# Performance work log

Measured on AMD Instinct MI355X. Metric: run time of the kernel, lower is better.

The kernel has to match this reference:

```python
import jax, jax.numpy as jnp
import numpy as np

N, DQ, T, H1 = 131072, 256, 4, 512

def setup_inputs() -> dict:
    key = jax.random.key(0)
    k_q, k_w0, k_b0, k_w1, k_z = jax.random.split(key, 5)
    return {
        "q": jax.random.normal(k_q, (N, DQ), dtype=jnp.float32),
        "Z": jax.random.randint(k_z, (N,), 0, T, dtype=jnp.int32),
        "W0": jax.random.normal(k_w0, (T, DQ, H1), dtype=jnp.float32) * (1.0 / np.sqrt(DQ)),
        "b0": jax.random.normal(k_b0, (T, H1), dtype=jnp.float32) * 0.01,
        "W1": jax.random.normal(k_w1, (T, H1), dtype=jnp.float32) * (1.0 / np.sqrt(H1)),
        "b1": jnp.zeros((), dtype=jnp.float32),
    }

def reference(q, Z, W0, b0, W1, b1):
    # Dense grouped-GEMM over all T types (T is small), then select per-atom
    # type result. Avoids materializing the per-atom [N, dq, h1] gathered
    # weight tensor that tf.gather would create.
    h_all = jnp.einsum('nd,tdh->nth', q, W0)              # [N, T, H1]
    h = jnp.take_along_axis(h_all, Z[:, None, None].astype(jnp.int32), axis=1)[:, 0, :]  # [N, H1]
    h = jnp.tanh(h + b0[Z])                               # hidden activations
    F = jnp.einsum('nh,nh->n', h, W1[Z]) + b1             # [N]
    return F
```

## Files before the change

### kernel.cpp

```cpp
#include <hip/hip_runtime.h>
#include <hip/hip_bf16.h>

#define N_ATOMS 131072
#define DQ 256
#define H1 512
#define NTYPES 4
#define TILE_M 64
#define NPAD (N_ATOMS + NTYPES * TILE_M)
#define MTILES ((N_ATOMS / TILE_M) + NTYPES)

typedef __bf16 bf16x8 __attribute__((ext_vector_type(8)));
typedef float f32x16 __attribute__((ext_vector_type(16)));

__device__ __forceinline__ unsigned short f2bf(float f) {
  unsigned int u = __builtin_bit_cast(unsigned int, f);
  u += 0x7fffu + ((u >> 16) & 1u);
  return (unsigned short)(u >> 16);
}

__device__ __forceinline__ float fast_tanh(float x) {
  float e = __expf(2.0f * x);
  return 1.0f - 2.0f * __builtin_amdgcn_rcpf(e + 1.0f);
}

__global__ __launch_bounds__(256) void prep_kernel(
    const float* __restrict__ W0, const int* __restrict__ Z,
    unsigned short* __restrict__ W0s, int* __restrict__ perm,
    int* __restrict__ blockcounts)
{
  const int b = blockIdx.x, tid = threadIdx.x;
  const int gid = b * 256 + tid;

  for (int i = gid; i < NPAD; i += 512 * 256) perm[i] = -1;

  if (gid < NTYPES * (DQ / 8) * H1) {
    const int n  = gid & (H1 - 1);
    const int kg = (gid >> 9) & 31;
    const int t  = gid >> 14;
    const float* src = W0 + ((size_t)(t * DQ + kg * 8) * H1 + n);
    unsigned short o[8];
#pragma unroll
    for (int j = 0; j < 8; ++j) o[j] = f2bf(src[(size_t)j * H1]);
    uint4 v;
    v.x = (unsigned)o[0] | ((unsigned)o[1] << 16);
    v.y = (unsigned)o[2] | ((unsigned)o[3] << 16);
    v.z = (unsigned)o[4] | ((unsigned)o[5] << 16);
    v.w = (unsigned)o[6] | ((unsigned)o[7] << 16);
    ((uint4*)W0s)[gid] = v;
  }

  __shared__ int lc[NTYPES];
  if (tid < NTYPES) lc[tid] = 0;
  __syncthreads();
  atomicAdd(&lc[Z[gid]], 1);
  __syncthreads();
  if (tid < NTYPES) blockcounts[b * NTYPES + tid] = lc[tid];
}

__global__ __launch_bounds__(256) void scan_kernel(
    const int* __restrict__ blockcounts, int* __restrict__ padded_off,
    int* __restrict__ cursors)
{
  __shared__ int sums[NTYPES];
  const int tid = threadIdx.x;
  if (tid < NTYPES) sums[tid] = 0;
  __syncthreads();
  const int t = tid & 3;
  int acc = 0;
  for (int b = tid >> 2; b < 512; b += 64) acc += blockcounts[b * 4 + t];
  atomicAdd(&sums[t], acc);
  __syncthreads();
  if (tid == 0) {
    int off = 0;
#pragma unroll
    for (int i = 0; i < NTYPES; ++i) {
      padded_off[i] = off;
      cursors[i] = off;
      off += (sums[i] + TILE_M - 1) & ~(TILE_M - 1);
    }
    padded_off[NTYPES] = off;
  }
}

__global__ __launch_bounds__(256) void scatter_kernel(
    const int* __restrict__ Z, int* __restrict__ cursors, int* __restrict__ perm)
{
  __shared__ int lc[NTYPES], lbase[NTYPES];
  const int tid = threadIdx.x;
  const int gid = blockIdx.x * 256 + tid;
  if (tid < NTYPES) lc[tid] = 0;
  __syncthreads();
  const int t  = Z[gid];
  const int my = atomicAdd(&lc[t], 1);
  __syncthreads();
  if (tid < NTYPES) lbase[tid] = lc[tid] ? atomicAdd(&cursors[tid], lc[tid]) : 0;
  __syncthreads();
  perm[lbase[t] + my] = gid;
}

__global__ __launch_bounds__(256, 2) void gemm_kernel(
    const float* __restrict__ q, const int* __restrict__ perm,
    const int* __restrict__ padded_off, const unsigned short* __restrict__ W0s,
    const float* __restrict__ b0, const float* __restrict__ W1,
    const float* __restrict__ b1p, float* __restrict__ out)
{
  __shared__ unsigned short Alds[(DQ / 8) * TILE_M * 8];
  __shared__ float Fws[4][TILE_M];

  const int gr0 = blockIdx.x * TILE_M;
  if (gr0 >= padded_off[NTYPES]) return;
  int t = 0;
#pragma unroll
  for (int i = 1; i < NTYPES; ++i) t += (gr0 >= padded_off[i]) ? 1 : 0;

  const int tid = threadIdx.x;

  {
    const int row = tid >> 2, c4 = tid & 3;
    const int atom = perm[gr0 + row];
    const float* qrow = q + (size_t)(atom < 0 ? 0 : atom) * DQ;
#pragma unroll
    for (int i = 0; i < 16; ++i) {
      const int k = c4 * 64 + i * 4;
      float4 v = make_float4(0.f, 0.f, 0.f, 0.f);
      if (atom >= 0) v = *(const float4*)(qrow + k);
      ushort4 o;
      o.x = f2bf(v.x); o.y = f2bf(v.y); o.z = f2bf(v.z); o.w = f2bf(v.w);
      *(ushort4*)&Alds[((k >> 3) * TILE_M + row) * 8 + (k & 7)] = o;
    }
  }
  __syncthreads();

  const int l = tid & 63, w = tid >> 6;
  const int half = l >> 5, ln = l & 31;

  f32x16 acc[2][4];
#pragma unroll
  for (int mt = 0; mt < 2; ++mt)
#pragma unroll
    for (int nt = 0; nt < 4; ++nt) acc[mt][nt] = (f32x16)0.0f;

  const unsigned short* Bt = W0s + (size_t)t * (DQ * H1);
  const unsigned short* Bbase = Bt + (size_t)(w * 128 + ln) * 8;

#pragma unroll 4
  for (int step = 0; step < 16; ++step) {
    const int kg = 2 * step + half;
    const bf16x8 a0 = *(const bf16x8*)&Alds[(kg * TILE_M + ln) * 8];
    const bf16x8 a1 = *(const bf16x8*)&Alds[(kg * TILE_M + 32 + ln) * 8];
    const unsigned short* bp = Bbase + (size_t)kg * (H1 * 8);
    const bf16x8 b0f = *(const bf16x8*)(bp);
    const bf16x8 b1f = *(const bf16x8*)(bp + 32 * 8);
    const bf16x8 b2f = *(const bf16x8*)(bp + 64 * 8);
    const bf16x8 b3f = *(const bf16x8*)(bp + 96 * 8);
    acc[0][0] = __builtin_amdgcn_mfma_f32_32x32x16_bf16(a0, b0f, acc[0][0], 0, 0, 0);
    acc[1][0] = __builtin_amdgcn_mfma_f32_32x32x16_bf16(a1, b0f, acc[1][0], 0, 0, 0);
    acc[0][1] = __builtin_amdgcn_mfma_f32_32x32x16_bf16(a0, b1f, acc[0][1], 0, 0, 0);
    acc[1][1] = __builtin_amdgcn_mfma_f32_32x32x16_bf16(a1, b1f, acc[1][1], 0, 0, 0);
    acc[0][2] = __builtin_amdgcn_mfma_f32_32x32x16_bf16(a0, b2f, acc[0][2], 0, 0, 0);
    acc[1][2] = __builtin_amdgcn_mfma_f32_32x32x16_bf16(a1, b2f, acc[1][2], 0, 0, 0);
    acc[0][3] = __builtin_amdgcn_mfma_f32_32x32x16_bf16(a0, b3f, acc[0][3], 0, 0, 0);
    acc[1][3] = __builtin_amdgcn_mfma_f32_32x32x16_bf16(a1, b3f, acc[1][3], 0, 0, 0);
  }

  float b0v[4], w1v[4];
#pragma unroll
  for (int nt = 0; nt < 4; ++nt) {
    const int c = w * 128 + nt * 32 + ln;
    b0v[nt] = b0[t * H1 + c];
    w1v[nt] = W1[t * H1 + c];
  }
#pragma unroll
  for (int mt = 0; mt < 2; ++mt) {
#pragma unroll
    for (int r = 0; r < 16; ++r) {
      float s = 0.f;
#pragma unroll
      for (int nt = 0; nt < 4; ++nt)
        s += w1v[nt] * fast_tanh(acc[mt][nt][r] + b0v[nt]);
      s += __shfl_xor(s, 1);
      s += __shfl_xor(s, 2);
      s += __shfl_xor(s, 4);
      s += __shfl_xor(s, 8);
      s += __shfl_xor(s, 16);
      if (ln == 0)
        Fws[w][mt * 32 + (r & 3) + 8 * (r >> 2) + 4 * half] = s;
    }
  }
  __syncthreads();

  if (tid < TILE_M) {
    const int atom = perm[gr0 + tid];
    if (atom >= 0)
      out[atom] = Fws[0][tid] + Fws[1][tid] + Fws[2][tid] + Fws[3][tid] + b1p[0];
  }
}

extern "C" void kernel_launch(void* const* d_in, const int* in_sizes, int n_in,
                              void* d_out, int out_size, void* d_ws, size_t ws_size,
                              hipStream_t stream) {
  const float* q  = (const float*)d_in[0];
  const int*   Z  = (const int*)d_in[1];
  const float* W0 = (const float*)d_in[2];
  const float* b0 = (const float*)d_in[3];
  const float* W1 = (const float*)d_in[4];
  const float* b1 = (const float*)d_in[5];
  float* out = (float*)d_out;

  char* ws = (char*)d_ws;
  int* blockcounts = (int*)(ws);
  int* padded_off  = (int*)(ws + 8192);
  int* cursors     = (int*)(ws + 8192 + 32);
  int* perm        = (int*)(ws + 8192 + 64);
  unsigned short* W0s = (unsigned short*)(ws + 8192 + 64 + (size_t)NPAD * 4);

  hipLaunchKernelGGL(prep_kernel,    dim3(512),    dim3(256), 0, stream, W0, Z, W0s, perm, blockcounts);
  hipLaunchKernelGGL(scan_kernel,    dim3(1),      dim3(256), 0, stream, blockcounts, padded_off, cursors);
  hipLaunchKernelGGL(scatter_kernel, dim3(512),    dim3(256), 0, stream, Z, cursors, perm);
  hipLaunchKernelGGL(gemm_kernel,    dim3(MTILES), dim3(256), 0, stream, q, perm, padded_off, W0s, b0, W1, b1, out);
}
```

Before: 281.4 us.

## Split GEMM N-dimension into two passes to cut accumulators and raise occupancy

```diff
diff --git a/kernel.cpp b/kernel.cpp
--- a/kernel.cpp
+++ b/kernel.cpp
@@ -98,14 +98,14 @@
   perm[lbase[t] + my] = gid;
 }
 
-__global__ __launch_bounds__(256, 2) void gemm_kernel(
+__global__ __launch_bounds__(256, 4) void gemm_kernel(
     const float* __restrict__ q, const int* __restrict__ perm,
     const int* __restrict__ padded_off, const unsigned short* __restrict__ W0s,
     const float* __restrict__ b0, const float* __restrict__ W1,
     const float* __restrict__ b1p, float* __restrict__ out)
 {
   __shared__ unsigned short Alds[(DQ / 8) * TILE_M * 8];
-  __shared__ float Fws[4][TILE_M];
+  __shared__ float Fws[16][TILE_M];
 
   const int gr0 = blockIdx.x * TILE_M;
   if (gr0 >= padded_off[NTYPES]) return;
@@ -134,65 +134,67 @@
   const int l = tid & 63, w = tid >> 6;
   const int half = l >> 5, ln = l & 31;
 
-  f32x16 acc[2][4];
-#pragma unroll
-  for (int mt = 0; mt < 2; ++mt)
-#pragma unroll
-    for (int nt = 0; nt < 4; ++nt) acc[mt][nt] = (f32x16)0.0f;
-
   const unsigned short* Bt = W0s + (size_t)t * (DQ * H1);
-  const unsigned short* Bbase = Bt + (size_t)(w * 128 + ln) * 8;
-
-#pragma unroll 4
-  for (int step = 0; step < 16; ++step) {
-    const int kg = 2 * step + half;
-    const bf16x8 a0 = *(const bf16x8*)&Alds[(kg * TILE_M + ln) * 8];
-    const bf16x8 a1 = *(const bf16x8*)&Alds[(kg * TILE_M + 32 + ln) * 8];
-    const unsigned short* bp = Bbase + (size_t)kg * (H1 * 8);
-    const bf16x8 b0f = *(const bf16x8*)(bp);
-    const bf16x8 b1f = *(const bf16x8*)(bp + 32 * 8);
-    const bf16x8 b2f = *(const bf16x8*)(bp + 64 * 8);
-    const bf16x8 b3f = *(const bf16x8*)(bp + 96 * 8);
-    acc[0][0] = __builtin_amdgcn_mfma_f32_32x32x16_bf16(a0, b0f, acc[0][0], 0, 0, 0);
-    acc[1][0] = __builtin_amdgcn_mfma_f32_32x32x16_bf16(a1, b0f, acc[1][0], 0, 0, 0);
-    acc[0][1] = __builtin_amdgcn_mfma_f32_32x32x16_bf16(a0, b1f, acc[0][1], 0, 0, 0);
-    acc[1][1] = __builtin_amdgcn_mfma_f32_32x32x16_bf16(a1, b1f, acc[1][1], 0, 0, 0);
-    acc[0][2] = __builtin_amdgcn_mfma_f32_32x32x16_bf16(a0, b2f, acc[0][2], 0, 0, 0);
-    acc[1][2] = __builtin_amdgcn_mfma_f32_32x32x16_bf16(a1, b2f, acc[1][2], 0, 0, 0);
-    acc[0][3] = __builtin_amdgcn_mfma_f32_32x32x16_bf16(a0, b3f, acc[0][3], 0, 0, 0);
-    acc[1][3] = __builtin_amdgcn_mfma_f32_32x32x16_bf16(a1, b3f, acc[1][3], 0, 0, 0);
-  }
-
-  float b0v[4], w1v[4];
-#pragma unroll
-  for (int nt = 0; nt < 4; ++nt) {
-    const int c = w * 128 + nt * 32 + ln;
-    b0v[nt] = b0[t * H1 + c];
-    w1v[nt] = W1[t * H1 + c];
-  }
-#pragma unroll
-  for (int mt = 0; mt < 2; ++mt) {
-#pragma unroll
-    for (int r = 0; r < 16; ++r) {
-      float s = 0.f;
-#pragma unroll
-      for (int nt = 0; nt < 4; ++nt)
-        s += w1v[nt] * fast_tanh(acc[mt][nt][r] + b0v[nt]);
-      s += __shfl_xor(s, 1);
-      s += __shfl_xor(s, 2);
-      s += __shfl_xor(s, 4);
-      s += __shfl_xor(s, 8);
-      s += __shfl_xor(s, 16);
-      if (ln == 0)
-        Fws[w][mt * 32 + (r & 3) + 8 * (r >> 2) + 4 * half] = s;
+
+#pragma unroll
+  for (int p = 0; p < 2; ++p) {
+    f32x16 acc[2][2];
+#pragma unroll
+    for (int mt = 0; mt < 2; ++mt)
+#pragma unroll
+      for (int nt = 0; nt < 2; ++nt) acc[mt][nt] = (f32x16)0.0f;
+
+    const unsigned short* Bbase = Bt + (size_t)(p * 256 + w * 64 + ln) * 8;
+
+#pragma unroll 2
+    for (int step = 0; step < 16; ++step) {
+      const int kg = 2 * step + half;
+      const bf16x8 a0 = *(const bf16x8*)&Alds[(kg * TILE_M + ln) * 8];
+      const bf16x8 a1 = *(const bf16x8*)&Alds[(kg * TILE_M + 32 + ln) * 8];
+      const unsigned short* bp = Bbase + (size_t)kg * (H1 * 8);
+      const bf16x8 bf0 = *(const bf16x8*)(bp);
+      const bf16x8 bf1 = *(const bf16x8*)(bp + 32 * 8);
+      acc[0][0] = __builtin_amdgcn_mfma_f32_32x32x16_bf16(a0, bf0, acc[0][0], 0, 0, 0);
+      acc[1][0] = __builtin_amdgcn_mfma_f32_32x32x16_bf16(a1, bf0, acc[1][0], 0, 0, 0);
+      acc[0][1] = __builtin_amdgcn_mfma_f32_32x32x16_bf16(a0, bf1, acc[0][1], 0, 0, 0);
+      acc[1][1] = __builtin_amdgcn_mfma_f32_32x32x16_bf16(a1, bf1, acc[1][1], 0, 0, 0);
+    }
+
+    float b0v[2], w1v[2];
+#pragma unroll
+    for (int nt = 0; nt < 2; ++nt) {
+      const int c = p * 256 + w * 64 + nt * 32 + ln;
+      b0v[nt] = b0[t * H1 + c];
+      w1v[nt] = W1[t * H1 + c];
+    }
+#pragma unroll
+    for (int mt = 0; mt < 2; ++mt) {
+#pragma unroll
+      for (int r = 0; r < 16; ++r) {
+        float s = w1v[0] * fast_tanh(acc[mt][0][r] + b0v[0])
+                + w1v[1] * fast_tanh(acc[mt][1][r] + b0v[1]);
+        s += __shfl_xor(s, 1);
+        s += __shfl_xor(s, 2);
+        s += __shfl_xor(s, 4);
+        if ((l & 7) == 0) {
+          const int row  = mt * 32 + (r & 3) + 8 * (r >> 2) + 4 * half;
+          const int slot = w * 4 + ((l >> 3) & 3);
+          if (p == 0) Fws[slot][row] = s;
+          else        Fws[slot][row] += s;
+        }
+      }
     }
   }
   __syncthreads();
 
   if (tid < TILE_M) {
     const int atom = perm[gr0 + tid];
-    if (atom >= 0)
-      out[atom] = Fws[0][tid] + Fws[1][tid] + Fws[2][tid] + Fws[3][tid] + b1p[0];
+    if (atom >= 0) {
+      float s = 0.f;
+#pragma unroll
+      for (int i = 0; i < 16; ++i) s += Fws[i][tid];
+      out[atom] = s + b1p[0];
+    }
   }
 }
 
```

Result: slower. 296.0 us (+5.2%).

## Add persistent double-buffered GEMM with async LDS loads of pre-converted bf16 q

Applied to the files above, without the earlier changes.

```diff
diff --git a/kernel.cpp b/kernel.cpp
--- a/kernel.cpp
+++ b/kernel.cpp
@@ -12,6 +12,13 @@
 typedef __bf16 bf16x8 __attribute__((ext_vector_type(8)));
 typedef float f32x16 __attribute__((ext_vector_type(16)));
 
+typedef __attribute__((address_space(3))) unsigned int lds_u32_t;
+typedef __attribute__((address_space(1))) const unsigned int glb_u32_t;
+
+__device__ __forceinline__ void async16(const void* g, void* l) {
+  __builtin_amdgcn_global_load_lds((glb_u32_t*)g, (lds_u32_t*)l, 16, 0, 0);
+}
+
 __device__ __forceinline__ unsigned short f2bf(float f) {
   unsigned int u = __builtin_bit_cast(unsigned int, f);
   u += 0x7fffu + ((u >> 16) & 1u);
@@ -24,9 +31,10 @@
 }
 
 __global__ __launch_bounds__(256) void prep_kernel(
-    const float* __restrict__ W0, const int* __restrict__ Z,
-    unsigned short* __restrict__ W0s, int* __restrict__ perm,
-    int* __restrict__ blockcounts)
+    const float* __restrict__ W0, const float* __restrict__ qf,
+    const int* __restrict__ Z, unsigned short* __restrict__ W0s,
+    unsigned short* __restrict__ qb, int* __restrict__ perm,
+    int* __restrict__ blockcounts, int qconv)
 {
   const int b = blockIdx.x, tid = threadIdx.x;
   const int gid = b * 256 + tid;
@@ -55,6 +63,15 @@
   atomicAdd(&lc[Z[gid]], 1);
   __syncthreads();
   if (tid < NTYPES) blockcounts[b * NTYPES + tid] = lc[tid];
+
+  if (qconv) {
+    for (int i = gid; i < (N_ATOMS * DQ) / 4; i += 512 * 256) {
+      const float4 v = ((const float4*)qf)[i];
+      ushort4 o;
+      o.x = f2bf(v.x); o.y = f2bf(v.y); o.z = f2bf(v.z); o.w = f2bf(v.w);
+      ((ushort4*)qb)[i] = o;
+    }
+  }
 }
 
 __global__ __launch_bounds__(256) void scan_kernel(
@@ -96,6 +113,119 @@
   if (tid < NTYPES) lbase[tid] = lc[tid] ? atomicAdd(&cursors[tid], lc[tid]) : 0;
   __syncthreads();
   perm[lbase[t] + my] = gid;
+}
+
+__global__ __launch_bounds__(256, 2) void gemm_persist(
+    const unsigned short* __restrict__ qb, const int* __restrict__ perm,
+    const int* __restrict__ padded_off, const unsigned short* __restrict__ W0s,
+    const float* __restrict__ b0, const float* __restrict__ W1,
+    const float* __restrict__ b1p, float* __restrict__ out)
+{
+  __shared__ unsigned short Alds[2][DQ / 8][TILE_M][8];
+  __shared__ float Fws[2][4][TILE_M];
+
+  const int tid = threadIdx.x;
+  const int l = tid & 63, w = tid >> 6;
+  const int half = l >> 5, ln = l & 31;
+  const int bx = (int)blockIdx.x;
+
+  const int po1 = padded_off[1], po2 = padded_off[2], po3 = padded_off[3];
+  const int po4 = padded_off[4];
+  const int NT = po4 / TILE_M;
+  const int ntile = 4 + ((bx < NT - 2048) ? 1 : 0);
+  const float b1v = b1p[0];
+
+  {
+    const int a0 = perm[bx * TILE_M + l];
+    const unsigned short* src = qb + (size_t)(a0 < 0 ? 0 : a0) * DQ;
+#pragma unroll
+    for (int i = 0; i < 8; ++i)
+      async16(src + (w * 8 + i) * 8, &Alds[0][w * 8 + i][0][0]);
+  }
+  int atomn = (ntile > 1) ? perm[(bx + 512) * TILE_M + l] : 0;
+  __syncthreads();
+
+  for (int it = 0; it < ntile; ++it) {
+    const int cur = it & 1;
+    const int tcur = (it < 4) ? bx + it * 512 : 2048 + bx;
+    const int gr0 = tcur * TILE_M;
+    const int t = ((gr0 >= po1) ? 1 : 0) + ((gr0 >= po2) ? 1 : 0)
+                + ((gr0 >= po3) ? 1 : 0);
+
+    f32x16 acc[2][4];
+#pragma unroll
+    for (int mt = 0; mt < 2; ++mt)
+#pragma unroll
+      for (int nt = 0; nt < 4; ++nt) acc[mt][nt] = (f32x16)0.0f;
+
+    const unsigned short* Bt = W0s + (size_t)t * (DQ * H1);
+    const unsigned short* Bbase = Bt + (size_t)(w * 128 + ln) * 8;
+
+#pragma unroll 4
+    for (int step = 0; step < 16; ++step) {
+      const int kg = 2 * step + half;
+      const bf16x8 a0 = *(const bf16x8*)&Alds[cur][kg][ln][0];
+      const bf16x8 a1 = *(const bf16x8*)&Alds[cur][kg][32 + ln][0];
+      const unsigned short* bp = Bbase + (size_t)kg * (H1 * 8);
+      const bf16x8 b0f = *(const bf16x8*)(bp);
+      const bf16x8 b1f = *(const bf16x8*)(bp + 32 * 8);
+      const bf16x8 b2f = *(const bf16x8*)(bp + 64 * 8);
+      const bf16x8 b3f = *(const bf16x8*)(bp + 96 * 8);
+      acc[0][0] = __builtin_amdgcn_mfma_f32_32x32x16_bf16(a0, b0f, acc[0][0], 0, 0, 0);
+      acc[1][0] = __builtin_amdgcn_mfma_f32_32x32x16_bf16(a1, b0f, acc[1][0], 0, 0, 0);
+      acc[0][1] = __builtin_amdgcn_mfma_f32_32x32x16_bf16(a0, b1f, acc[0][1], 0, 0, 0);
+      acc[1][1] = __builtin_amdgcn_mfma_f32_32x32x16_bf16(a1, b1f, acc[1][1], 0, 0, 0);
+      acc[0][2] = __builtin_amdgcn_mfma_f32_32x32x16_bf16(a0, b2f, acc[0][2], 0, 0, 0);
+      acc[1][2] = __builtin_amdgcn_mfma_f32_32x32x16_bf16(a1, b2f, acc[1][2], 0, 0, 0);
+      acc[0][3] = __builtin_amdgcn_mfma_f32_32x32x16_bf16(a0, b3f, acc[0][3], 0, 0, 0);
+      acc[1][3] = __builtin_amdgcn_mfma_f32_32x32x16_bf16(a1, b3f, acc[1][3], 0, 0, 0);
+    }
+
+    float b0v[4], w1v[4];
+#pragma unroll
+    for (int nt = 0; nt < 4; ++nt) {
+      const int c = w * 128 + nt * 32 + ln;
+      b0v[nt] = b0[t * H1 + c];
+      w1v[nt] = W1[t * H1 + c];
+    }
+
+    if (it + 1 < ntile) {
+      const unsigned short* srcn = qb + (size_t)(atomn < 0 ? 0 : atomn) * DQ;
+#pragma unroll
+      for (int i = 0; i < 8; ++i)
+        async16(srcn + (w * 8 + i) * 8, &Alds[cur ^ 1][w * 8 + i][0][0]);
+      if (it + 2 < ntile) {
+        const int tnn = (it + 2 < 4) ? bx + (it + 2) * 512 : 2048 + bx;
+        atomn = perm[tnn * TILE_M + l];
+      }
+    }
+
+#pragma unroll
+    for (int mt = 0; mt < 2; ++mt) {
+#pragma unroll
+      for (int r = 0; r < 16; ++r) {
+        float s = 0.f;
+#pragma unroll
+        for (int nt = 0; nt < 4; ++nt)
+          s += w1v[nt] * fast_tanh(acc[mt][nt][r] + b0v[nt]);
+        s += __shfl_xor(s, 1);
+        s += __shfl_xor(s, 2);
+        s += __shfl_xor(s, 4);
+        s += __shfl_xor(s, 8);
+        s += __shfl_xor(s, 16);
+        if (ln == 0)
+          Fws[cur][w][mt * 32 + (r & 3) + 8 * (r >> 2) + 4 * half] = s;
+      }
+    }
+    __syncthreads();
+
+    if (tid < TILE_M) {
+      const int a = perm[gr0 + tid];
+      if (a >= 0)
+        out[a] = Fws[cur][0][tid] + Fws[cur][1][tid] + Fws[cur][2][tid]
+               + Fws[cur][3][tid] + b1v;
+    }
+  }
 }
 
 __global__ __launch_bounds__(256, 2) void gemm_kernel(
@@ -114,7 +244,6 @@
   for (int i = 1; i < NTYPES; ++i) t += (gr0 >= padded_off[i]) ? 1 : 0;
 
   const int tid = threadIdx.x;
-
   {
     const int row = tid >> 2, c4 = tid & 3;
     const int atom = perm[gr0 + row];
@@ -214,8 +343,22 @@
   int* perm        = (int*)(ws + 8192 + 64);
   unsigned short* W0s = (unsigned short*)(ws + 8192 + 64 + (size_t)NPAD * 4);
 
-  hipLaunchKernelGGL(prep_kernel,    dim3(512),    dim3(256), 0, stream, W0, Z, W0s, perm, blockcounts);
-  hipLaunchKernelGGL(scan_kernel,    dim3(1),      dim3(256), 0, stream, blockcounts, padded_off, cursors);
-  hipLaunchKernelGGL(scatter_kernel, dim3(512),    dim3(256), 0, stream, Z, cursors, perm);
-  hipLaunchKernelGGL(gemm_kernel,    dim3(MTILES), dim3(256), 0, stream, q, perm, padded_off, W0s, b0, W1, b1, out);
-}
+  const size_t qb_off = ((8192 + 64 + (size_t)NPAD * 4
+                        + (size_t)NTYPES * DQ * H1 * 2) + 511) & ~(size_t)511;
+  const size_t need = qb_off + (size_t)N_ATOMS * DQ * 2;
+  const int use_persist = (ws_size >= need) ? 1 : 0;
+  unsigned short* qb = (unsigned short*)(ws + qb_off);
+
+  hipLaunchKernelGGL(prep_kernel, dim3(512), dim3(256), 0, stream,
+                     W0, q, Z, W0s, qb, perm, blockcounts, use_persist);
+  hipLaunchKernelGGL(scan_kernel, dim3(1), dim3(256), 0, stream,
+                     blockcounts, padded_off, cursors);
+  hipLaunchKernelGGL(scatter_kernel, dim3(512), dim3(256), 0, stream,
+                     Z, cursors, perm);
+  if (use_persist)
+    hipLaunchKernelGGL(gemm_persist, dim3(512), dim3(256), 0, stream,
+                       qb, perm, padded_off, W0s, b0, W1, b1, out);
+  else
+    hipLaunchKernelGGL(gemm_kernel, dim3(MTILES), dim3(256), 0, stream,
+                       q, perm, padded_off, W0s, b0, W1, b1, out);
+}
```

After: 303.6 us. +7.9%, slower.

## Merge bucketing kernels and make GEMM persistent with double-buffered tile prefetch

Applied to the files above, without the earlier changes.

```diff
diff --git a/kernel.cpp b/kernel.cpp
--- a/kernel.cpp
+++ b/kernel.cpp
@@ -6,8 +6,6 @@
 #define H1 512
 #define NTYPES 4
 #define TILE_M 64
-#define NPAD (N_ATOMS + NTYPES * TILE_M)
-#define MTILES ((N_ATOMS / TILE_M) + NTYPES)
 
 typedef __bf16 bf16x8 __attribute__((ext_vector_type(8)));
 typedef float f32x16 __attribute__((ext_vector_type(16)));
@@ -23,15 +21,17 @@
   return 1.0f - 2.0f * __builtin_amdgcn_rcpf(e + 1.0f);
 }
 
+__global__ __launch_bounds__(64) void init_kernel(int* __restrict__ hdr) {
+  if (threadIdx.x < 16) hdr[threadIdx.x] = 0;
+}
+
 __global__ __launch_bounds__(256) void prep_kernel(
     const float* __restrict__ W0, const int* __restrict__ Z,
     unsigned short* __restrict__ W0s, int* __restrict__ perm,
-    int* __restrict__ blockcounts)
+    int* __restrict__ cnt)
 {
   const int b = blockIdx.x, tid = threadIdx.x;
   const int gid = b * 256 + tid;
-
-  for (int i = gid; i < NPAD; i += 512 * 256) perm[i] = -1;
 
   if (gid < NTYPES * (DQ / 8) * H1) {
     const int n  = gid & (H1 - 1);
@@ -49,151 +49,176 @@
     ((uint4*)W0s)[gid] = v;
   }
 
-  __shared__ int lc[NTYPES];
-  if (tid < NTYPES) lc[tid] = 0;
-  __syncthreads();
-  atomicAdd(&lc[Z[gid]], 1);
-  __syncthreads();
-  if (tid < NTYPES) blockcounts[b * NTYPES + tid] = lc[tid];
-}
-
-__global__ __launch_bounds__(256) void scan_kernel(
-    const int* __restrict__ blockcounts, int* __restrict__ padded_off,
-    int* __restrict__ cursors)
-{
-  __shared__ int sums[NTYPES];
-  const int tid = threadIdx.x;
-  if (tid < NTYPES) sums[tid] = 0;
-  __syncthreads();
-  const int t = tid & 3;
-  int acc = 0;
-  for (int b = tid >> 2; b < 512; b += 64) acc += blockcounts[b * 4 + t];
-  atomicAdd(&sums[t], acc);
-  __syncthreads();
-  if (tid == 0) {
-    int off = 0;
-#pragma unroll
-    for (int i = 0; i < NTYPES; ++i) {
-      padded_off[i] = off;
-      cursors[i] = off;
-      off += (sums[i] + TILE_M - 1) & ~(TILE_M - 1);
-    }
-    padded_off[NTYPES] = off;
-  }
-}
-
-__global__ __launch_bounds__(256) void scatter_kernel(
-    const int* __restrict__ Z, int* __restrict__ cursors, int* __restrict__ perm)
-{
   __shared__ int lc[NTYPES], lbase[NTYPES];
-  const int tid = threadIdx.x;
-  const int gid = blockIdx.x * 256 + tid;
   if (tid < NTYPES) lc[tid] = 0;
   __syncthreads();
   const int t  = Z[gid];
   const int my = atomicAdd(&lc[t], 1);
   __syncthreads();
-  if (tid < NTYPES) lbase[tid] = lc[tid] ? atomicAdd(&cursors[tid], lc[tid]) : 0;
-  __syncthreads();
-  perm[lbase[t] + my] = gid;
-}
-
-__global__ __launch_bounds__(256, 2) void gemm_kernel(
+  if (tid < NTYPES) lbase[tid] = lc[tid] ? atomicAdd(&cnt[tid], lc[tid]) : 0;
+  __syncthreads();
+  perm[t * N_ATOMS + lbase[t] + my] = gid;
+}
+
+__device__ __forceinline__ void issue_loads(float4* st, const float* q,
+                                            int atom, int c4) {
+  const float* qrow = q + (size_t)atom * DQ + c4 * 64;
+#pragma unroll
+  for (int i = 0; i < 16; ++i) st[i] = *(const float4*)(qrow + i * 4);
+}
+
+__device__ __forceinline__ void convert_store(
+    const float4* st, unsigned short (*A)[TILE_M][8], int row, int c4) {
+#pragma unroll
+  for (int i2 = 0; i2 < 8; ++i2) {
+    const int k = c4 * 64 + i2 * 8;
+    uint4 vv;
+    vv.x = (unsigned)f2bf(st[2*i2].x)     | ((unsigned)f2bf(st[2*i2].y)   << 16);
+    vv.y = (unsigned)f2bf(st[2*i2].z)     | ((unsigned)f2bf(st[2*i2].w)   << 16);
+    vv.z = (unsigned)f2bf(st[2*i2+1].x)   | ((unsigned)f2bf(st[2*i2+1].y) << 16);
+    vv.w = (unsigned)f2bf(st[2*i2+1].z)   | ((unsigned)f2bf(st[2*i2+1].w) << 16);
+    *(uint4*)&A[k >> 3][row][0] = vv;
+  }
+}
+
+__global__ __launch_bounds__(256, 2) void gemm_persist(
     const float* __restrict__ q, const int* __restrict__ perm,
-    const int* __restrict__ padded_off, const unsigned short* __restrict__ W0s,
-    const float* __restrict__ b0, const float* __restrict__ W1,
+    const int* __restrict__ cnt, int* __restrict__ ticket,
+    const unsigned short* __restrict__ W0s,
+    const float* __restrict__ b0g, const float* __restrict__ W1,
     const float* __restrict__ b1p, float* __restrict__ out)
 {
-  __shared__ unsigned short Alds[(DQ / 8) * TILE_M * 8];
-  __shared__ float Fws[4][TILE_M];
-
-  const int gr0 = blockIdx.x * TILE_M;
-  if (gr0 >= padded_off[NTYPES]) return;
-  int t = 0;
-#pragma unroll
-  for (int i = 1; i < NTYPES; ++i) t += (gr0 >= padded_off[i]) ? 1 : 0;
+  __shared__ unsigned short Alds[2][DQ / 8][TILE_M][8];
+  __shared__ float Fws[2][4][TILE_M];
+  __shared__ int shvt[2];
 
   const int tid = threadIdx.x;
-
-  {
-    const int row = tid >> 2, c4 = tid & 3;
-    const int atom = perm[gr0 + row];
-    const float* qrow = q + (size_t)(atom < 0 ? 0 : atom) * DQ;
-#pragma unroll
-    for (int i = 0; i < 16; ++i) {
-      const int k = c4 * 64 + i * 4;
-      float4 v = make_float4(0.f, 0.f, 0.f, 0.f);
-      if (atom >= 0) v = *(const float4*)(qrow + k);
-      ushort4 o;
-      o.x = f2bf(v.x); o.y = f2bf(v.y); o.z = f2bf(v.z); o.w = f2bf(v.w);
-      *(ushort4*)&Alds[((k >> 3) * TILE_M + row) * 8 + (k & 7)] = o;
-    }
-  }
-  __syncthreads();
-
   const int l = tid & 63, w = tid >> 6;
   const int half = l >> 5, ln = l & 31;
-
-  f32x16 acc[2][4];
-#pragma unroll
-  for (int mt = 0; mt < 2; ++mt)
-#pragma unroll
-    for (int nt = 0; nt < 4; ++nt) acc[mt][nt] = (f32x16)0.0f;
-
-  const unsigned short* Bt = W0s + (size_t)t * (DQ * H1);
-  const unsigned short* Bbase = Bt + (size_t)(w * 128 + ln) * 8;
-
+  const int row = tid >> 2, c4 = tid & 3;
+
+  const int c0 = cnt[0], c1 = cnt[1], c2 = cnt[2], c3 = cnt[3];
+  const int n0 = (c0 + 63) >> 6, n1 = (c1 + 63) >> 6;
+  const int n2 = (c2 + 63) >> 6, n3 = (c3 + 63) >> 6;
+  const int p1 = n0, p2 = n0 + n1, p3 = n0 + n1 + n2;
+  const int total = n0 + n1 + n2 + n3;
+  const float b1v = b1p[0];
+
+#define DECODE(v, T, J0, CT) do {                                   \
+    T = ((v) >= p1) + ((v) >= p2) + ((v) >= p3);                    \
+    const int pre_ = (T == 0) ? 0 : (T == 1) ? p1 : (T == 2) ? p2 : p3; \
+    CT = (T == 0) ? c0 : (T == 1) ? c1 : (T == 2) ? c2 : c3;        \
+    J0 = ((v) - pre_) * TILE_M; } while (0)
+
+  int vt_cur = (int)blockIdx.x;
+  int t_cur, j0_cur, ct_cur;
+  DECODE(vt_cur, t_cur, j0_cur, ct_cur);
+
+  float4 st[16];
+  {
+    int atom = 0;
+    if (j0_cur + row < ct_cur) atom = perm[t_cur * N_ATOMS + j0_cur + row];
+    issue_loads(st, q, atom, c4);
+  }
+  convert_store(st, Alds[0], row, c4);
+  if (tid == 0) shvt[0] = 512 + atomicAdd(ticket, 1);
+  __syncthreads();
+
+  int vt_nxt = shvt[0];
+  int t_nxt = 0, j0_nxt = 0, ct_nxt = 0, anext = 0;
+  if (vt_nxt < total) {
+    DECODE(vt_nxt, t_nxt, j0_nxt, ct_nxt);
+    if (j0_nxt + row < ct_nxt) anext = perm[t_nxt * N_ATOMS + j0_nxt + row];
+  }
+  int cur = 0, par = 0;
+
+  while (vt_cur < total) {
+    f32x16 acc[2][4];
+#pragma unroll
+    for (int mt = 0; mt < 2; ++mt)
+#pragma unroll
+      for (int nt = 0; nt < 4; ++nt) acc[mt][nt] = (f32x16)0.0f;
+
+    const unsigned short* Bt = W0s + (size_t)t_cur * (DQ * H1);
+    const unsigned short* Bbase = Bt + (size_t)(w * 128 + ln) * 8;
+
+    __builtin_amdgcn_s_setprio(1);
 #pragma unroll 4
-  for (int step = 0; step < 16; ++step) {
-    const int kg = 2 * step + half;
-    const bf16x8 a0 = *(const bf16x8*)&Alds[(kg * TILE_M + ln) * 8];
-    const bf16x8 a1 = *(const bf16x8*)&Alds[(kg * TILE_M + 32 + ln) * 8];
-    const unsigned short* bp = Bbase + (size_t)kg * (H1 * 8);
-    const bf16x8 b0f = *(const bf16x8*)(bp);
-    const bf16x8 b1f = *(const bf16x8*)(bp + 32 * 8);
-    const bf16x8 b2f = *(const bf16x8*)(bp + 64 * 8);
-    const bf16x8 b3f = *(const bf16x8*)(bp + 96 * 8);
-    acc[0][0] = __builtin_amdgcn_mfma_f32_32x32x16_bf16(a0, b0f, acc[0][0], 0, 0, 0);
-    acc[1][0] = __builtin_amdgcn_mfma_f32_32x32x16_bf16(a1, b0f, acc[1][0], 0, 0, 0);
-    acc[0][1] = __builtin_amdgcn_mfma_f32_32x32x16_bf16(a0, b1f, acc[0][1], 0, 0, 0);
-    acc[1][1] = __builtin_amdgcn_mfma_f32_32x32x16_bf16(a1, b1f, acc[1][1], 0, 0, 0);
-    acc[0][2] = __builtin_amdgcn_mfma_f32_32x32x16_bf16(a0, b2f, acc[0][2], 0, 0, 0);
-    acc[1][2] = __builtin_amdgcn_mfma_f32_32x32x16_bf16(a1, b2f, acc[1][2], 0, 0, 0);
-    acc[0][3] = __builtin_amdgcn_mfma_f32_32x32x16_bf16(a0, b3f, acc[0][3], 0, 0, 0);
-    acc[1][3] = __builtin_amdgcn_mfma_f32_32x32x16_bf16(a1, b3f, acc[1][3], 0, 0, 0);
-  }
-
-  float b0v[4], w1v[4];
-#pragma unroll
-  for (int nt = 0; nt < 4; ++nt) {
-    const int c = w * 128 + nt * 32 + ln;
-    b0v[nt] = b0[t * H1 + c];
-    w1v[nt] = W1[t * H1 + c];
-  }
-#pragma unroll
-  for (int mt = 0; mt < 2; ++mt) {
-#pragma unroll
-    for (int r = 0; r < 16; ++r) {
-      float s = 0.f;
-#pragma unroll
-      for (int nt = 0; nt < 4; ++nt)
-        s += w1v[nt] * fast_tanh(acc[mt][nt][r] + b0v[nt]);
-      s += __shfl_xor(s, 1);
-      s += __shfl_xor(s, 2);
-      s += __shfl_xor(s, 4);
-      s += __shfl_xor(s, 8);
-      s += __shfl_xor(s, 16);
-      if (ln == 0)
-        Fws[w][mt * 32 + (r & 3) + 8 * (r >> 2) + 4 * half] = s;
-    }
-  }
-  __syncthreads();
-
-  if (tid < TILE_M) {
-    const int atom = perm[gr0 + tid];
-    if (atom >= 0)
-      out[atom] = Fws[0][tid] + Fws[1][tid] + Fws[2][tid] + Fws[3][tid] + b1p[0];
-  }
+    for (int step = 0; step < 16; ++step) {
+      const int kg = 2 * step + half;
+      const bf16x8 a0 = *(const bf16x8*)&Alds[cur][kg][ln][0];
+      const bf16x8 a1 = *(const bf16x8*)&Alds[cur][kg][32 + ln][0];
+      const unsigned short* bp = Bbase + (size_t)kg * (H1 * 8);
+      const bf16x8 b0f = *(const bf16x8*)(bp);
+      const bf16x8 b1f = *(const bf16x8*)(bp + 32 * 8);
+      const bf16x8 b2f = *(const bf16x8*)(bp + 64 * 8);
+      const bf16x8 b3f = *(const bf16x8*)(bp + 96 * 8);
+      acc[0][0] = __builtin_amdgcn_mfma_f32_32x32x16_bf16(a0, b0f, acc[0][0], 0, 0, 0);
+      acc[1][0] = __builtin_amdgcn_mfma_f32_32x32x16_bf16(a1, b0f, acc[1][0], 0, 0, 0);
+      acc[0][1] = __builtin_amdgcn_mfma_f32_32x32x16_bf16(a0, b1f, acc[0][1], 0, 0, 0);
+      acc[1][1] = __builtin_amdgcn_mfma_f32_32x32x16_bf16(a1, b1f, acc[1][1], 0, 0, 0);
+      acc[0][2] = __builtin_amdgcn_mfma_f32_32x32x16_bf16(a0, b2f, acc[0][2], 0, 0, 0);
+      acc[1][2] = __builtin_amdgcn_mfma_f32_32x32x16_bf16(a1, b2f, acc[1][2], 0, 0, 0);
+      acc[0][3] = __builtin_amdgcn_mfma_f32_32x32x16_bf16(a0, b3f, acc[0][3], 0, 0, 0);
+      acc[1][3] = __builtin_amdgcn_mfma_f32_32x32x16_bf16(a1, b3f, acc[1][3], 0, 0, 0);
+    }
+    __builtin_amdgcn_s_setprio(0);
+
+    const bool have_nxt = (vt_nxt < total);
+    if (have_nxt) issue_loads(st, q, anext, c4);
+
+    float b0v[4], w1v[4];
+#pragma unroll
+    for (int nt = 0; nt < 4; ++nt) {
+      const int c = w * 128 + nt * 32 + ln;
+      b0v[nt] = b0g[t_cur * H1 + c];
+      w1v[nt] = W1[t_cur * H1 + c];
+    }
+
+#pragma unroll
+    for (int mt = 0; mt < 2; ++mt) {
+#pragma unroll
+      for (int r = 0; r < 16; ++r) {
+        float s = 0.f;
+#pragma unroll
+        for (int nt = 0; nt < 4; ++nt)
+          s += w1v[nt] * fast_tanh(acc[mt][nt][r] + b0v[nt]);
+        s += __shfl_xor(s, 1);
+        s += __shfl_xor(s, 2);
+        s += __shfl_xor(s, 4);
+        s += __shfl_xor(s, 8);
+        s += __shfl_xor(s, 16);
+        if (ln == 0)
+          Fws[cur][w][mt * 32 + (r & 3) + 8 * (r >> 2) + 4 * half] = s;
+      }
+    }
+
+    if (have_nxt) convert_store(st, Alds[cur ^ 1], row, c4);
+
+    if (tid == 0 && have_nxt) shvt[par ^ 1] = 512 + atomicAdd(ticket, 1);
+
+    __syncthreads();
+
+    if (tid < TILE_M && j0_cur + tid < ct_cur) {
+      const int a = perm[t_cur * N_ATOMS + j0_cur + tid];
+      out[a] = Fws[cur][0][tid] + Fws[cur][1][tid] + Fws[cur][2][tid]
+             + Fws[cur][3][tid] + b1v;
+    }
+
+    if (have_nxt) {
+      vt_cur = vt_nxt; t_cur = t_nxt; j0_cur = j0_nxt; ct_cur = ct_nxt;
+      vt_nxt = shvt[par ^ 1];
+      anext = 0;
+      if (vt_nxt < total) {
+        DECODE(vt_nxt, t_nxt, j0_nxt, ct_nxt);
+        if (j0_nxt + row < ct_nxt) anext = perm[t_nxt * N_ATOMS + j0_nxt + row];
+      }
+    } else {
+      vt_cur = total;
+    }
+    cur ^= 1; par ^= 1;
+  }
+#undef DECODE
 }
 
 extern "C" void kernel_launch(void* const* d_in, const int* in_sizes, int n_in,
@@ -208,14 +233,16 @@
   float* out = (float*)d_out;
 
   char* ws = (char*)d_ws;
-  int* blockcounts = (int*)(ws);
-  int* padded_off  = (int*)(ws + 8192);
-  int* cursors     = (int*)(ws + 8192 + 32);
-  int* perm        = (int*)(ws + 8192 + 64);
-  unsigned short* W0s = (unsigned short*)(ws + 8192 + 64 + (size_t)NPAD * 4);
-
-  hipLaunchKernelGGL(prep_kernel,    dim3(512),    dim3(256), 0, stream, W0, Z, W0s, perm, blockcounts);
-  hipLaunchKernelGGL(scan_kernel,    dim3(1),      dim3(256), 0, stream, blockcounts, padded_off, cursors);
-  hipLaunchKernelGGL(scatter_kernel, dim3(512),    dim3(256), 0, stream, Z, cursors, perm);
-  hipLaunchKernelGGL(gemm_kernel,    dim3(MTILES), dim3(256), 0, stream, q, perm, padded_off, W0s, b0, W1, b1, out);
-}
+  int* hdr    = (int*)(ws);
+  int* cnt    = hdr;
+  int* ticket = hdr + 4;
+  int* perm   = (int*)(ws + 64);
+  unsigned short* W0s =
+      (unsigned short*)(ws + 64 + (size_t)NTYPES * N_ATOMS * 4);
+
+  hipLaunchKernelGGL(init_kernel, dim3(1), dim3(64), 0, stream, hdr);
+  hipLaunchKernelGGL(prep_kernel, dim3(512), dim3(256), 0, stream,
+                     W0, Z, W0s, perm, cnt);
+  hipLaunchKernelGGL(gemm_persist, dim3(512), dim3(256), 0, stream,
+                     q, perm, cnt, ticket, W0s, b0, W1, b1, out);
+}
```

Result: slower. 300.5 us (+6.8%).
